# Kernel optimization log

Hardware: AMD Instinct MI355X
Metric: run time of the kernel (lower is better)

The kernel has to match this reference:

```python
import jax, jax.numpy as jnp
import numpy as np

B, S, H, NH = 2, 2048, 1024, 16
HD = H // NH  # head_dim = 64


def setup_inputs() -> dict:
    key = jax.random.key(0)
    k1, k2, k3 = jax.random.split(key, 3)
    x = jax.random.normal(k1, (B, S, H), dtype=jnp.float32)
    # additive causal mask: 0 on/below diagonal, -1e9 above
    causal = jnp.tril(jnp.ones((S, S), dtype=bool))
    mask = jnp.where(causal, 0.0, -1e9).astype(jnp.float32)[None, None, :, :]
    # fan-in scaled init like flax Dense default (lecun_normal)
    W_qkv = jax.random.normal(k2, (H, 3 * H), dtype=jnp.float32) / np.sqrt(H)
    W_out = jax.random.normal(k3, (H, H), dtype=jnp.float32) / np.sqrt(H)
    return {"x": x, "mask": mask, "W_qkv": W_qkv, "W_out": W_out}


def reference(x, mask, W_qkv, W_out):
    b, s, _ = x.shape
    qkv = jnp.einsum('bsh,hf->bsf', x, W_qkv)  # [B,S,3H]
    q, k, v = jnp.split(qkv, 3, axis=-1)
    q = q.reshape(b, s, NH, HD)
    k = k.reshape(b, s, NH, HD)
    v = v.reshape(b, s, NH, HD)
    scores = jnp.einsum('bqhd,bkhd->bhqk', q, k) / jnp.sqrt(jnp.float32(HD))
    scores = scores + mask
    attn = jax.nn.softmax(scores, axis=-1)
    y = jnp.einsum('bhqk,bkhd->bqhd', attn, v).reshape(b, s, H)
    return jnp.einsum('bsh,ho->bso', y, W_out)
```

## Files before the change

kernel.cpp:

```cpp
#include <hip/hip_runtime.h>

#define B_ 2
#define S_ 2048
#define H_ 1024
#define NH_ 16
#define HD_ 64

typedef short s16x8 __attribute__((ext_vector_type(8)));
typedef float f32x4 __attribute__((ext_vector_type(4)));

__device__ __forceinline__ ushort f2bf(float f) {
  union { float f; unsigned u; } v;
  v.f = f;
  unsigned r = (v.u + 0x7fffu + ((v.u >> 16) & 1u)) >> 16;
  return (ushort)r;
}

__device__ __forceinline__ void gload16(const void* g, void* l) {
  typedef const __attribute__((address_space(1))) unsigned int* gp_t;
  typedef __attribute__((address_space(3))) unsigned int* lp_t;
  __builtin_amdgcn_global_load_lds((gp_t)g, (lp_t)l, 16, 0, 0);
}

__global__ __launch_bounds__(256) void k_convert(const float* __restrict__ in,
                                                 ushort* __restrict__ out) {
  int i = blockIdx.x * 256 + threadIdx.x;
  float4 v = ((const float4*)in)[i];
  ushort4 o;
  o.x = f2bf(v.x); o.y = f2bf(v.y); o.z = f2bf(v.z); o.w = f2bf(v.w);
  ((ushort4*)out)[i] = o;
}

__global__ __launch_bounds__(256) void k_transpose(const float* __restrict__ in,
                                                   ushort* __restrict__ out,
                                                   int R, int C) {
  __shared__ ushort tile[32][33];
  int c0 = blockIdx.x * 32, r0 = blockIdx.y * 32;
  int tr = threadIdx.x >> 5, tc = threadIdx.x & 31;
#pragma unroll
  for (int i = 0; i < 4; ++i)
    tile[tr + 8 * i][tc] = f2bf(in[(size_t)(r0 + tr + 8 * i) * C + c0 + tc]);
  __syncthreads();
#pragma unroll
  for (int i = 0; i < 4; ++i)
    out[(size_t)(c0 + tr + 8 * i) * R + r0 + tc] = tile[tc][tr + 8 * i];
}

template <int MODE>
__global__ __launch_bounds__(256) void k_gemm(const ushort* __restrict__ A,
                                              const ushort* __restrict__ Bt,
                                              void* __restrict__ out0,
                                              ushort* __restrict__ outK,
                                              ushort* __restrict__ outV,
                                              int Kdim, int Ndim) {
  __shared__ __align__(16) ushort As[128 * 64];
  __shared__ __align__(16) ushort Bs[128 * 64];
  const int nwg = gridDim.x * gridDim.y;
  const int id = blockIdx.y * gridDim.x + blockIdx.x;
  const int sid = (id & 7) * (nwg >> 3) + (id >> 3);
  const int m0 = (sid / gridDim.x) * 128, n0 = (sid % gridDim.x) * 128;
  const int tid = threadIdx.x, lane = tid & 63, w = tid >> 6;
  const int g = lane >> 4, c = lane & 15;
  const int wr = w >> 1, wc = w & 1;
  f32x4 acc[4][4] = {};
  const int trow = tid >> 3, tcol = tid & 7;
  const ushort* ag = A + (size_t)(m0 + trow) * Kdim + tcol * 8;
  const ushort* bg = Bt + (size_t)(n0 + trow) * Kdim + tcol * 8;
  ushort* la = As + tid * 8;
  ushort* lb = Bs + tid * 8;

  for (int k0 = 0; k0 < Kdim; k0 += 64) {
#pragma unroll
    for (int i = 0; i < 4; ++i) {
      gload16(ag + k0 + i * 32 * Kdim, la + i * 2048);
      gload16(bg + k0 + i * 32 * Kdim, lb + i * 2048);
    }
    __syncthreads();
#pragma unroll
    for (int kk = 0; kk < 64; kk += 32) {
      s16x8 af[4], bfr[4];
#pragma unroll
      for (int i = 0; i < 4; ++i)
        af[i] = *(const s16x8*)(As + (wr * 64 + i * 16 + c) * 64 + kk + g * 8);
#pragma unroll
      for (int i = 0; i < 4; ++i)
        bfr[i] = *(const s16x8*)(Bs + (wc * 64 + i * 16 + c) * 64 + kk + g * 8);
#pragma unroll
      for (int i = 0; i < 4; ++i)
#pragma unroll
        for (int j = 0; j < 4; ++j)
          acc[i][j] = __builtin_amdgcn_mfma_f32_16x16x32_bf16(af[i], bfr[j], acc[i][j], 0, 0, 0);
    }
    __syncthreads();
  }

  if (MODE == 1) {
    float* out = (float*)out0;
#pragma unroll
    for (int i = 0; i < 4; ++i) {
      int mb = m0 + wr * 64 + i * 16 + g * 4;
#pragma unroll
      for (int j = 0; j < 4; ++j) {
        int n = n0 + wc * 64 + j * 16 + c;
#pragma unroll
        for (int r = 0; r < 4; ++r)
          out[(size_t)(mb + r) * Ndim + n] = acc[i][j][r];
      }
    }
  } else {
    if (n0 < 1024) {
      const float ALPHA = 0.18033688f;
      ushort* outQ = (ushort*)out0;
#pragma unroll
      for (int i = 0; i < 4; ++i) {
        int mb = m0 + wr * 64 + i * 16 + g * 4;
#pragma unroll
        for (int j = 0; j < 4; ++j) {
          int n = n0 + wc * 64 + j * 16 + c;
#pragma unroll
          for (int r = 0; r < 4; ++r)
            outQ[(size_t)(mb + r) * 1024 + n] = f2bf(acc[i][j][r] * ALPHA);
        }
      }
    } else if (n0 < 2048) {
#pragma unroll
      for (int i = 0; i < 4; ++i) {
        int mb = m0 + wr * 64 + i * 16 + g * 4;
#pragma unroll
        for (int j = 0; j < 4; ++j) {
          int n = n0 - 1024 + wc * 64 + j * 16 + c;
#pragma unroll
          for (int r = 0; r < 4; ++r)
            outK[(size_t)(mb + r) * 1024 + n] = f2bf(acc[i][j][r]);
        }
      }
    } else {
#pragma unroll
      for (int i = 0; i < 4; ++i) {
        int mb = m0 + wr * 64 + i * 16 + g * 4;
        int bidx = mb >> 11;
        int s = mb & 2047;
#pragma unroll
        for (int j = 0; j < 4; ++j) {
          int nv = n0 - 2048 + wc * 64 + j * 16 + c;
          int h = nv >> 6, d = nv & 63;
          ushort4 pk;
          pk.x = f2bf(acc[i][j][0]);
          pk.y = f2bf(acc[i][j][1]);
          pk.z = f2bf(acc[i][j][2]);
          pk.w = f2bf(acc[i][j][3]);
          *(ushort4*)(outV + ((size_t)((bidx * 16 + h) * 64 + d)) * 2048 + s) = pk;
        }
      }
    }
  }
}

__global__ __launch_bounds__(256) void k_attn(const ushort* __restrict__ Qb,
                                              const ushort* __restrict__ Kb,
                                              const ushort* __restrict__ Vt,
                                              ushort* __restrict__ Yb) {
  __shared__ __align__(16) ushort Ks[2][64 * 64];
  __shared__ __align__(16) ushort Vs[2][64 * 64];
  __shared__ __align__(16) unsigned int Pp[4][16 * 32];
  const int fid = blockIdx.x;
  const int wid = (fid & 7) * 64 + (fid >> 3);
  const int bh = wid >> 4;
  const int j = wid & 15;
  const int b = bh >> 4, h = bh & 15;
  const int tid = threadIdx.x, w = tid >> 6, lane = tid & 63;
  const int g = lane >> 4, c = lane & 15;
  char* pb = (char*)(&Pp[w][0]);

  const int trow = tid >> 3, tcol = tid & 7;
  const int csrc = tcol ^ (trow & 7);
  const ushort* kgb = Kb + (size_t)(b * S_ + trow) * H_ + h * HD_ + csrc * 8;
  const ushort* vgb = Vt + (size_t)(bh * HD_ + trow) * S_ + csrc * 8;

#define STAGE(bf, tile)                                          \
  do {                                                           \
    int ks_ = (tile) * 64;                                       \
    gload16(kgb + (size_t)ks_ * H_, Ks[bf] + tid * 8);           \
    gload16(kgb + (size_t)(ks_ + 32) * H_, Ks[bf] + 2048 + tid * 8); \
    gload16(vgb + ks_, Vs[bf] + tid * 8);                        \
    gload16(vgb + ks_ + 32 * S_, Vs[bf] + 2048 + tid * 8);       \
  } while (0)

#pragma unroll 1
  for (int half = 0; half < 2; ++half) {
    const int qc = half ? (31 - j) : j;
    const int q0 = qc * 64;
    const int nt = qc + 1;
    const int qw = q0 + w * 16;

    s16x8 qf[2];
#pragma unroll
    for (int dc = 0; dc < 2; ++dc)
      qf[dc] = *(const s16x8*)(Qb + (size_t)(b * S_ + qw + c) * H_ +
                               h * HD_ + dc * 32 + g * 8);

    f32x4 oacc[4] = {};
    float m = -1e30f, lp = 0.f;

    STAGE(0, 0);
    asm volatile("s_waitcnt vmcnt(0)" ::: "memory");
    __builtin_amdgcn_s_barrier();
    __builtin_amdgcn_sched_barrier(0);

    int buf = 0;
#pragma unroll 1
    for (int it = 0; it < nt; ++it) {
      const int ks = it * 64;
      if (it + 1 < nt) STAGE(buf ^ 1, it + 1);

      f32x4 sacc[4] = {};
      __builtin_amdgcn_s_setprio(1);
#pragma unroll
      for (int dc = 0; dc < 2; ++dc) {
#pragma unroll
        for (int kt = 0; kt < 4; ++kt) {
          int R = kt * 16 + c;
          int cc = dc * 4 + g;
          s16x8 kf = *(const s16x8*)((const char*)Ks[buf] + R * 128 + ((cc ^ (R & 7)) << 4));
          sacc[kt] = __builtin_amdgcn_mfma_f32_16x16x32_bf16(kf, qf[dc], sacc[kt], 0, 0, 0);
        }
      }
      __builtin_amdgcn_s_setprio(0);

      if (it == nt - 1) {
        int q = qw + c;
#pragma unroll
        for (int kt = 0; kt < 4; ++kt)
#pragma unroll
          for (int r = 0; r < 4; ++r)
            if (ks + kt * 16 + g * 4 + r > q) sacc[kt][r] = -1e30f;
      }

      float t0 = fmaxf(fmaxf(sacc[0][0], sacc[0][1]), fmaxf(sacc[0][2], sacc[0][3]));
      float t1 = fmaxf(fmaxf(sacc[1][0], sacc[1][1]), fmaxf(sacc[1][2], sacc[1][3]));
      float t2 = fmaxf(fmaxf(sacc[2][0], sacc[2][1]), fmaxf(sacc[2][2], sacc[2][3]));
      float t3 = fmaxf(fmaxf(sacc[3][0], sacc[3][1]), fmaxf(sacc[3][2], sacc[3][3]));
      float t = fmaxf(fmaxf(t0, t1), fmaxf(t2, t3));
      t = fmaxf(t, __shfl_xor(t, 16));
      t = fmaxf(t, __shfl_xor(t, 32));

      if (__any(t > m + 8.0f)) {
        float mnew = fmaxf(m, t);
        float sc = __builtin_amdgcn_exp2f(m - mnew);
        m = mnew;
        lp *= sc;
        float scq[4];
#pragma unroll
        for (int r = 0; r < 4; ++r) scq[r] = __shfl(sc, g * 4 + r);
#pragma unroll
        for (int dt = 0; dt < 4; ++dt)
#pragma unroll
          for (int r = 0; r < 4; ++r) oacc[dt][r] *= scq[r];
      }

      float p[4][4];
      float rs = 0.f;
#pragma unroll
      for (int kt = 0; kt < 4; ++kt)
#pragma unroll
        for (int r = 0; r < 4; ++r) {
          p[kt][r] = __builtin_amdgcn_exp2f(sacc[kt][r] - m);
          rs += p[kt][r];
        }
      lp += rs;
      unsigned int pw[8];
#pragma unroll
      for (int kt = 0; kt < 4; ++kt) {
        asm("v_cvt_pk_bf16_f32 %0, %1, %2" : "=v"(pw[kt * 2 + 0]) : "v"(p[kt][0]), "v"(p[kt][1]));
        asm("v_cvt_pk_bf16_f32 %0, %1, %2" : "=v"(pw[kt * 2 + 1]) : "v"(p[kt][2]), "v"(p[kt][3]));
      }
#pragma unroll
      for (int kt = 0; kt < 4; ++kt) {
        int qd = kt * 2 + (g >> 1);
        *(uint2*)(pb + c * 128 + ((qd ^ (c & 7)) << 4) + ((g & 1) << 3)) =
            make_uint2(pw[kt * 2], pw[kt * 2 + 1]);
      }
      asm volatile("s_waitcnt lgkmcnt(0)" ::: "memory");
      __builtin_amdgcn_sched_barrier(0);

      __builtin_amdgcn_s_setprio(1);
#pragma unroll
      for (int kc = 0; kc < 2; ++kc) {
        int qd = kc * 4 + g;
        s16x8 pf = *(const s16x8*)(pb + c * 128 + ((qd ^ (c & 7)) << 4));
        int cc = kc * 4 + g;
#pragma unroll
        for (int dt = 0; dt < 4; ++dt) {
          int R = dt * 16 + c;
          s16x8 vf = *(const s16x8*)((const char*)Vs[buf] + R * 128 + ((cc ^ (R & 7)) << 4));
          oacc[dt] = __builtin_amdgcn_mfma_f32_16x16x32_bf16(pf, vf, oacc[dt], 0, 0, 0);
        }
      }
      __builtin_amdgcn_s_setprio(0);

      asm volatile("s_waitcnt vmcnt(0)" ::: "memory");
      __builtin_amdgcn_s_barrier();
      __builtin_amdgcn_sched_barrier(0);
      buf ^= 1;
    }

    float lt = lp;
    lt += __shfl_xor(lt, 16);
    lt += __shfl_xor(lt, 32);
    float rq[4];
#pragma unroll
    for (int r = 0; r < 4; ++r) rq[r] = 1.0f / __shfl(lt, g * 4 + r);
#pragma unroll
    for (int dt = 0; dt < 4; ++dt)
#pragma unroll
      for (int r = 0; r < 4; ++r) {
        int s = qw + g * 4 + r;
        Yb[(size_t)(b * S_ + s) * H_ + h * HD_ + dt * 16 + c] = f2bf(oacc[dt][r] * rq[r]);
      }
  }
#undef STAGE
}

extern "C" void kernel_launch(void* const* d_in, const int* in_sizes, int n_in,
                              void* d_out, int out_size, void* d_ws, size_t ws_size,
                              hipStream_t stream) {
  (void)in_sizes; (void)n_in; (void)out_size; (void)ws_size;
  const float* x = (const float*)d_in[0];
  const float* Wqkv = (const float*)d_in[2];
  const float* Wout = (const float*)d_in[3];
  float* out = (float*)d_out;

  char* ws = (char*)d_ws;
  ushort* xb    = (ushort*)(ws + 0);
  ushort* wqkvT = (ushort*)(ws + 8388608);
  ushort* woutT = (ushort*)(ws + 14680064);
  ushort* Qb    = (ushort*)(ws + 16777216);
  ushort* Kb    = (ushort*)(ws + 25165824);
  ushort* Vtb   = (ushort*)(ws + 33554432);
  ushort* Yb    = (ushort*)(ws + 41943040);

  k_convert<<<dim3(4096), dim3(256), 0, stream>>>(x, xb);
  k_transpose<<<dim3(96, 32), dim3(256), 0, stream>>>(Wqkv, wqkvT, 1024, 3072);
  k_transpose<<<dim3(32, 32), dim3(256), 0, stream>>>(Wout, woutT, 1024, 1024);
  k_gemm<0><<<dim3(24, 32), dim3(256), 0, stream>>>(xb, wqkvT, (void*)Qb, Kb, Vtb, 1024, 3072);
  k_attn<<<dim3(512), dim3(256), 0, stream>>>(Qb, Kb, Vtb, Yb);
  k_gemm<1><<<dim3(8, 32), dim3(256), 0, stream>>>(Yb, woutT, (void*)out, nullptr, nullptr, 1024, 1024);
}
```

Before: 216.1 us.

## Double-buffer GEMM LDS tiles and fuse convert/transpose prep kernels

The GEMM kernel now keeps two LDS buffers for A and B, so it can issue global-to-LDS loads for the next K tile while running MFMAs on the current one. This replaces the load-sync-compute-sync loop and hides global load latency. It also raises MFMA wave priority during compute. Separately, the x conversion and the two weight transposes are merged into one launch to save launch overhead. The cost is twice the LDS use per block (64KB), which can lower occupancy.

```diff
diff --git a/kernel.cpp b/kernel.cpp
--- a/kernel.cpp
+++ b/kernel.cpp
@@ -22,20 +22,29 @@
   __builtin_amdgcn_global_load_lds((gp_t)g, (lp_t)l, 16, 0, 0);
 }
 
-__global__ __launch_bounds__(256) void k_convert(const float* __restrict__ in,
-                                                 ushort* __restrict__ out) {
-  int i = blockIdx.x * 256 + threadIdx.x;
-  float4 v = ((const float4*)in)[i];
-  ushort4 o;
-  o.x = f2bf(v.x); o.y = f2bf(v.y); o.z = f2bf(v.z); o.w = f2bf(v.w);
-  ((ushort4*)out)[i] = o;
-}
-
-__global__ __launch_bounds__(256) void k_transpose(const float* __restrict__ in,
-                                                   ushort* __restrict__ out,
-                                                   int R, int C) {
+__global__ __launch_bounds__(256) void k_prep(const float* __restrict__ x,
+                                              ushort* __restrict__ xb,
+                                              const float* __restrict__ Wqkv,
+                                              ushort* __restrict__ wqkvT,
+                                              const float* __restrict__ Wout,
+                                              ushort* __restrict__ woutT) {
   __shared__ ushort tile[32][33];
-  int c0 = blockIdx.x * 32, r0 = blockIdx.y * 32;
+  const int bid = blockIdx.x;
+  if (bid < 4096) {
+    int i = bid * 256 + threadIdx.x;
+    float4 v = ((const float4*)x)[i];
+    ushort4 o;
+    o.x = f2bf(v.x); o.y = f2bf(v.y); o.z = f2bf(v.z); o.w = f2bf(v.w);
+    ((ushort4*)xb)[i] = o;
+    return;
+  }
+  const float* in;
+  ushort* out;
+  int R = 1024, C, t;
+  if (bid < 7168) { in = Wqkv; out = wqkvT; C = 3072; t = bid - 4096; }
+  else            { in = Wout; out = woutT; C = 1024; t = bid - 7168; }
+  int nbx = C >> 5;
+  int c0 = (t % nbx) * 32, r0 = (t / nbx) * 32;
   int tr = threadIdx.x >> 5, tc = threadIdx.x & 31;
 #pragma unroll
   for (int i = 0; i < 4; ++i)
@@ -53,8 +62,8 @@
                                               ushort* __restrict__ outK,
                                               ushort* __restrict__ outV,
                                               int Kdim, int Ndim) {
-  __shared__ __align__(16) ushort As[128 * 64];
-  __shared__ __align__(16) ushort Bs[128 * 64];
+  __shared__ __align__(16) ushort As[2][128 * 64];
+  __shared__ __align__(16) ushort Bs[2][128 * 64];
   const int nwg = gridDim.x * gridDim.y;
   const int id = blockIdx.y * gridDim.x + blockIdx.x;
   const int sid = (id & 7) * (nwg >> 3) + (id >> 3);
@@ -66,33 +75,48 @@
   const int trow = tid >> 3, tcol = tid & 7;
   const ushort* ag = A + (size_t)(m0 + trow) * Kdim + tcol * 8;
   const ushort* bg = Bt + (size_t)(n0 + trow) * Kdim + tcol * 8;
-  ushort* la = As + tid * 8;
-  ushort* lb = Bs + tid * 8;
-
-  for (int k0 = 0; k0 < Kdim; k0 += 64) {
-#pragma unroll
-    for (int i = 0; i < 4; ++i) {
-      gload16(ag + k0 + i * 32 * Kdim, la + i * 2048);
-      gload16(bg + k0 + i * 32 * Kdim, lb + i * 2048);
-    }
-    __syncthreads();
+
+#define STAGE_G(bf, k0)                                      \
+  do {                                                       \
+    _Pragma("unroll") for (int i_ = 0; i_ < 4; ++i_) {       \
+      gload16(ag + (k0) + i_ * 32 * Kdim, As[bf] + tid * 8 + i_ * 2048); \
+      gload16(bg + (k0) + i_ * 32 * Kdim, Bs[bf] + tid * 8 + i_ * 2048); \
+    }                                                        \
+  } while (0)
+
+  const int nk = Kdim >> 6;
+  STAGE_G(0, 0);
+  asm volatile("s_waitcnt vmcnt(0)" ::: "memory");
+  __builtin_amdgcn_s_barrier();
+  __builtin_amdgcn_sched_barrier(0);
+
+  int buf = 0;
+#pragma unroll 1
+  for (int t = 0; t < nk; ++t) {
+    if (t + 1 < nk) STAGE_G(buf ^ 1, (t + 1) * 64);
 #pragma unroll
     for (int kk = 0; kk < 64; kk += 32) {
       s16x8 af[4], bfr[4];
 #pragma unroll
       for (int i = 0; i < 4; ++i)
-        af[i] = *(const s16x8*)(As + (wr * 64 + i * 16 + c) * 64 + kk + g * 8);
+        af[i] = *(const s16x8*)(As[buf] + (wr * 64 + i * 16 + c) * 64 + kk + g * 8);
 #pragma unroll
       for (int i = 0; i < 4; ++i)
-        bfr[i] = *(const s16x8*)(Bs + (wc * 64 + i * 16 + c) * 64 + kk + g * 8);
+        bfr[i] = *(const s16x8*)(Bs[buf] + (wc * 64 + i * 16 + c) * 64 + kk + g * 8);
+      __builtin_amdgcn_s_setprio(1);
 #pragma unroll
       for (int i = 0; i < 4; ++i)
 #pragma unroll
         for (int j = 0; j < 4; ++j)
           acc[i][j] = __builtin_amdgcn_mfma_f32_16x16x32_bf16(af[i], bfr[j], acc[i][j], 0, 0, 0);
+      __builtin_amdgcn_s_setprio(0);
     }
-    __syncthreads();
+    asm volatile("s_waitcnt vmcnt(0)" ::: "memory");
+    __builtin_amdgcn_s_barrier();
+    __builtin_amdgcn_sched_barrier(0);
+    buf ^= 1;
   }
+#undef STAGE_G
 
   if (MODE == 1) {
     float* out = (float*)out0;
@@ -339,9 +363,7 @@
   ushort* Vtb   = (ushort*)(ws + 33554432);
   ushort* Yb    = (ushort*)(ws + 41943040);
 
-  k_convert<<<dim3(4096), dim3(256), 0, stream>>>(x, xb);
-  k_transpose<<<dim3(96, 32), dim3(256), 0, stream>>>(Wqkv, wqkvT, 1024, 3072);
-  k_transpose<<<dim3(32, 32), dim3(256), 0, stream>>>(Wout, woutT, 1024, 1024);
+  k_prep<<<dim3(8192), dim3(256), 0, stream>>>(x, xb, Wqkv, wqkvT, Wout, woutT);
   k_gemm<0><<<dim3(24, 32), dim3(256), 0, stream>>>(xb, wqkvT, (void*)Qb, Kb, Vtb, 1024, 3072);
   k_attn<<<dim3(512), dim3(256), 0, stream>>>(Qb, Kb, Vtb, Yb);
   k_gemm<1><<<dim3(8, 32), dim3(256), 0, stream>>>(Yb, woutT, (void*)out, nullptr, nullptr, 1024, 1024);
```

Result: faster. 209.5 us (-3.0%).
